# Kernel tuning notes

Hardware: AMD Instinct MI355X
Metric: run time of the kernel (lower is better)

Reference implementation:

```python
import jax, jax.numpy as jnp
import numpy as np

N, D, K = 65536, 256, 4096
INIT_COUNT = 100  # torch: counts = ones(K, int32) * 100


def setup_inputs() -> dict:
    key = jax.random.key(0)
    k1, k2 = jax.random.split(key)
    embedded = jax.random.normal(k1, (N, D), dtype=jnp.float32)
    centers = jax.random.normal(k2, (K, D), dtype=jnp.float32)
    counts = jnp.full((K,), INIT_COUNT, dtype=jnp.int32)
    return {"embedded": embedded, "centers": centers, "counts": counts}


def reference(embedded, centers, counts):
    # --- predict_hard: squared euclidean distance [N,K] + argmin ---
    x2 = jnp.sum(embedded * embedded, axis=1, keepdims=True)       # [N,1]
    c2 = jnp.sum(centers * centers, axis=1)                        # [K]
    d2 = x2 - 2.0 * (embedded @ centers.T) + c2                    # [N,K]
    labels = jnp.argmin(d2, axis=1).astype(jnp.int32)              # [N]

    # --- dcn_loss: mean over batch of squared dist to assigned center ---
    loss = jnp.sum((embedded - centers[labels]) ** 2) / embedded.shape[0]

    # --- update_centroids: sequential running-mean update, closed form ---
    # c <- (1-1/n)c + (1/n)x repeated over assigned samples collapses to
    # (count0 * c0 + sum_assigned x) / (count0 + m)
    seg_sum = jax.ops.segment_sum(embedded, labels, num_segments=K)            # [K,D]
    seg_cnt = jax.ops.segment_sum(
        jnp.ones((embedded.shape[0],), dtype=embedded.dtype), labels, num_segments=K
    )                                                                           # [K]
    c0 = counts.astype(embedded.dtype)                                          # [K]
    new_centers = (c0[:, None] * centers + seg_sum) / (c0 + seg_cnt)[:, None]  # [K,D]
    new_counts = counts + seg_cnt.astype(jnp.int32)                             # [K]
    return labels, new_centers, new_counts, loss
```

## Files before the change

### kernel.cpp

```cpp
#include <hip/hip_runtime.h>
#include <cfloat>
#include <cstdint>

constexpr int N  = 65536;
constexpr int D  = 256;
constexpr int K  = 4096;

typedef __attribute__((ext_vector_type(8))) _Float16 half8;
typedef __attribute__((ext_vector_type(8))) unsigned short ushort8;
typedef __attribute__((ext_vector_type(4))) float floatx4;

__device__ __forceinline__ floatx4 mfma_f16(half8 a, half8 b, floatx4 c) {
    return __builtin_amdgcn_mfma_f32_16x16x32_f16(a, b, c, 0, 0, 0);
}

__device__ __forceinline__ void ld_lds16(void* lds, const void* g) {
    __builtin_amdgcn_global_load_lds(
        (const __attribute__((address_space(1))) unsigned int*)g,
        (__attribute__((address_space(3))) unsigned int*)lds, 16, 0, 0);
}

__global__ void prep_c2(const float* __restrict__ C, float* __restrict__ c2) {
    int k = blockIdx.x;
    int l = threadIdx.x;
    const float4* row = (const float4*)(C + (size_t)k * D);
    float4 v = row[l];
    float s = v.x*v.x + v.y*v.y + v.z*v.z + v.w*v.w;
    #pragma unroll
    for (int m = 1; m < 64; m <<= 1) s += __shfl_xor(s, m);
    if (l == 0) c2[k] = s;
}

__global__ void convert_f16_both(const float* __restrict__ X, const float* __restrict__ C,
                                 unsigned short* __restrict__ Xh,
                                 unsigned short* __restrict__ Ch,
                                 float* __restrict__ xsq_part,
                                 float* __restrict__ c2) {
    __shared__ float red[4];
    int id = blockIdx.x * 256 + threadIdx.x;
    const int nX = N * D / 8;
    bool isX = id < nX;
    const float* src; unsigned short* dst;
    if (isX) { src = X; dst = Xh; }
    else     { src = C; dst = Ch; id -= nX; }
    const float4* s4 = (const float4*)src;
    float4 a = s4[2*id], b = s4[2*id+1];
    float xs[8] = {a.x,a.y,a.z,a.w,b.x,b.y,b.z,b.w};
    ushort8 h;
    float ps = 0.f;
    #pragma unroll
    for (int i = 0; i < 8; ++i) {
        union { _Float16 f; unsigned short u; } cv;
        cv.f = (_Float16)xs[i];
        h[i] = cv.u;
        ps += xs[i]*xs[i];
    }
    ((ushort8*)dst)[id] = h;
    int t = threadIdx.x;
    if (isX) {
        #pragma unroll
        for (int m = 1; m < 64; m <<= 1) ps += __shfl_xor(ps, m);
        if ((t & 63) == 0) red[t >> 6] = ps;
        __syncthreads();
        if (t == 0) xsq_part[blockIdx.x] = (red[0] + red[1]) + (red[2] + red[3]);
    } else {
        #pragma unroll
        for (int m = 1; m < 32; m <<= 1) ps += __shfl_xor(ps, m);
        if ((t & 31) == 0) c2[id >> 5] = ps;
    }
}

__global__ __launch_bounds__(256, 3) void mfma_assign(
        const unsigned short* __restrict__ Xh, const unsigned short* __restrict__ Ch,
        const float* __restrict__ c2g, float* __restrict__ cand)
{
    __shared__ __align__(16) unsigned short sA[2*8192];
    __shared__ __align__(16) unsigned short sB[2*4096];
    __shared__ float sC2[1024];

    const int t    = threadIdx.x;
    const int w    = t >> 6, l = t & 63;
    const int quad = l >> 4, lr = l & 15;

    const int bid   = blockIdx.x;
    const int sw    = (bid & 7) * 256 + (bid >> 3);
    const int kb    = sw & 3;
    const int panel = sw >> 2;
    const int rowbase = panel * 128;

    const int rl  = l >> 2;
    const int gsw = (l & 3) ^ ((l >> 3) & 3);

    ((float4*)sC2)[t] = ((const float4*)(c2g + kb*1024))[t];

#define STAGE(nk, db) do {                                                     \
        _Pragma("unroll")                                                      \
        for (int m_ = 0; m_ < 4; ++m_) {                                       \
            int dkk_ = m_ & 1, q_ = 2*w + (m_ >> 1);                           \
            const unsigned short* gp_ = Xh + (size_t)(rowbase + q_*16 + rl)*D  \
                + (((nk) & 3)*2 + dkk_)*32 + gsw*8;                            \
            ld_lds16((char*)sA + (db)*16384 + dkk_*8192 + q_*1024, gp_);       \
        }                                                                      \
        _Pragma("unroll")                                                      \
        for (int dkk_ = 0; dkk_ < 2; ++dkk_) {                                 \
            const unsigned short* gp_ = Ch + (size_t)(kb*1024 + ((nk)>>2)*64   \
                + w*16 + rl)*D + (((nk) & 3)*2 + dkk_)*32 + gsw*8;             \
            ld_lds16((char*)sB + (db)*8192 + dkk_*4096 + w*1024, gp_);         \
        }                                                                      \
    } while (0)

    STAGE(0, 0);

    const char* sAc = (const char*)sA;
    const char* sBc = (const char*)sB;
    const int slot   = quad ^ ((lr >> 1) & 3);
    const int sA_off = ((32*w + lr)*4 + slot)*16;
    const int sB_off = (lr*4 + slot)*16;

#define KSTEP(dkk) do {                                                        \
        const char* aB_ = sAc + buf*16384 + (dkk)*8192;                        \
        const char* bB_ = sBc + buf*8192  + (dkk)*4096;                        \
        half8 Af0 = *(const half8*)(aB_ + 0*1024 + sA_off);                    \
        half8 Af1 = *(const half8*)(aB_ + 1*1024 + sA_off);                    \
        half8 Bf0 = *(const half8*)(bB_ + 0*1024 + sB_off);                    \
        half8 Bf1 = *(const half8*)(bB_ + 1*1024 + sB_off);                    \
        half8 Bf2 = *(const half8*)(bB_ + 2*1024 + sB_off);                    \
        half8 Bf3 = *(const half8*)(bB_ + 3*1024 + sB_off);                    \
        acc[0][0] = mfma_f16(Af0, Bf0, acc[0][0]);                             \
        acc[1][0] = mfma_f16(Af1, Bf0, acc[1][0]);                             \
        acc[0][1] = mfma_f16(Af0, Bf1, acc[0][1]);                             \
        acc[1][1] = mfma_f16(Af1, Bf1, acc[1][1]);                             \
        acc[0][2] = mfma_f16(Af0, Bf2, acc[0][2]);                             \
        acc[1][2] = mfma_f16(Af1, Bf2, acc[1][2]);                             \
        acc[0][3] = mfma_f16(Af0, Bf3, acc[0][3]);                             \
        acc[1][3] = mfma_f16(Af1, Bf3, acc[1][3]);                             \
    } while (0)

#define FLUSH(h) do {                                                          \
    _Pragma("unroll")                                                          \
    for (int i = 0; i < 2; ++i)                                                \
        _Pragma("unroll")                                                      \
        for (int r = 0; r < 4; ++r) {                                          \
            int st = 4*i + r;                                                  \
            float a1 = v1[st], a2 = v2[st]; int ax1 = x1[st], ax2 = x2s[st];   \
            _Pragma("unroll")                                                  \
            for (int m = 1; m < 16; m <<= 1) {                                 \
                float b1f = __shfl_xor(a1, m); int bx1 = __shfl_xor(ax1, m);   \
                float b2f = __shfl_xor(a2, m); int bx2 = __shfl_xor(ax2, m);   \
                bool tt = (b1f < a1) || (b1f == a1 && bx1 < ax1);              \
                float n1 = tt ? b1f : a1; int nx1 = tt ? bx1 : ax1;            \
                float w1 = tt ? a1 : b1f; int wx1 = tt ? ax1 : bx1;            \
                float w2 = tt ? b2f : a2; int wx2 = tt ? bx2 : ax2;            \
                bool uu = (w2 < w1) || (w2 == w1 && wx2 < wx1);                \
                a1 = n1; ax1 = nx1;                                            \
                a2 = uu ? w2 : w1; ax2 = uu ? wx2 : wx1;                       \
            }                                                                  \
            if (lr == 0) {                                                     \
                int row = rowbase + 32*w + 16*i + 4*quad + r;                  \
                float4 o; o.x = a1; o.y = __int_as_float(ax1);                 \
                o.z = a2; o.w = __int_as_float(ax2);                           \
                ((float4*)cand)[(size_t)row*8 + (h)] = o;                      \
            }                                                                  \
            v1[st] = FLT_MAX; v2[st] = FLT_MAX;                                \
            x1[st] = 0x7fffffff; x2s[st] = 0x7fffffff;                         \
        } } while (0)

    float v1[8], v2[8]; int x1[8], x2s[8];
    #pragma unroll
    for (int i = 0; i < 8; ++i) { v1[i]=FLT_MAX; v2[i]=FLT_MAX; x1[i]=0x7fffffff; x2s[i]=0x7fffffff; }

    floatx4 acc[2][4];
    float c2v[4]; int jidx[4];
    int buf = 0;

    for (int ks = 0; ks < 64; ++ks) {
        __syncthreads();

        if (ks < 63) STAGE(ks + 1, buf ^ 1);

        if ((ks & 3) == 0) {
            const int ct = ks >> 2;
            #pragma unroll
            for (int i = 0; i < 2; ++i)
                #pragma unroll
                for (int j = 0; j < 4; ++j) acc[i][j] = (floatx4)0.f;
            #pragma unroll
            for (int j = 0; j < 4; ++j) {
                int cc = ct*64 + 16*j + lr;
                c2v[j] = sC2[cc];
                jidx[j] = kb*1024 + cc;
            }
        }

        KSTEP(0);
        KSTEP(1);

        if ((ks & 3) == 3) {
            #pragma unroll
            for (int i = 0; i < 2; ++i)
                #pragma unroll
                for (int j = 0; j < 4; ++j)
                    #pragma unroll
                    for (int r = 0; r < 4; ++r) {
                        float s = fmaf(-2.f, acc[i][j][r], c2v[j]);
                        int st = 4*i + r;
                        bool cA = s < v1[st];
                        bool cB = s < v2[st];
                        float tv = cB ? s : v2[st]; int tx = cB ? jidx[j] : x2s[st];
                        v2[st] = cA ? v1[st] : tv;  x2s[st] = cA ? x1[st] : tx;
                        v1[st] = cA ? s : v1[st];   x1[st]  = cA ? jidx[j] : x1[st];
                    }
        }
        if (ks == 31) FLUSH(2*kb);
        buf ^= 1;
    }
    FLUSH(2*kb + 1);

#undef STAGE
#undef KSTEP
#undef FLUSH
}

__global__ __launch_bounds__(256) void recheck_label(
        const float* __restrict__ X, const float* __restrict__ C,
        const float* __restrict__ c2, const float* __restrict__ cand,
        float* __restrict__ out_labels, int* __restrict__ labInt,
        int* __restrict__ cnt)
{
    int t = threadIdx.x, w = t >> 6, l = t & 63;
    int g  = l >> 4;
    int lr = l & 15;
    int row0 = (blockIdx.x * 4 + w) * 4;
    int row  = row0 + g;

    float4 e = ((const float4*)cand)[(size_t)row*8 + (lr >> 1)];
    float s  = (lr & 1) ? e.z : e.x;
    int  idx = (lr & 1) ? __float_as_int(e.w) : __float_as_int(e.y);

    float a1 = s, a2 = FLT_MAX; int ax1 = idx, ax2 = 0x7fffffff;
    #pragma unroll
    for (int m = 1; m < 16; m <<= 1) {
        float b1 = __shfl_xor(a1, m); int bx1 = __shfl_xor(ax1, m);
        float b2 = __shfl_xor(a2, m); int bx2 = __shfl_xor(ax2, m);
        bool tt = (b1 < a1) || (b1 == a1 && bx1 < ax1);
        float n1 = tt ? b1 : a1; int nx1 = tt ? bx1 : ax1;
        float w1 = tt ? a1 : b1; int wx1 = tt ? ax1 : bx1;
        float w2 = tt ? b2 : a2; int wx2 = tt ? bx2 : ax2;
        bool uu = (w2 < w1) || (w2 == w1 && wx2 < wx1);
        a1 = n1; ax1 = nx1;
        a2 = uu ? w2 : w1; ax2 = uu ? wx2 : wx1;
    }

    bool certain = (a2 - a1 > 0.25f);
    unsigned long long certMask = __ballot(certain);

    if (certain && lr == 0) {
        out_labels[row] = (float)ax1;
        labInt[row] = ax1;
        atomicAdd(&cnt[ax1], 1);
    }

    #pragma unroll
    for (int q = 0; q < 4; ++q) {
        if ((certMask >> (q*16)) & 1ull) continue;
        int r = row0 + q;
        float sq  = __shfl(s,   q*16 + lr);
        int   iq  = __shfl(idx, q*16 + lr);
        float gs1 = __shfl(a1,  q*16);

        float4 xv = ((const float4*)X)[(size_t)r*64 + l];
        float px = xv.x*xv.x + xv.y*xv.y + xv.z*xv.z + xv.w*xv.w;
        #pragma unroll
        for (int m = 1; m < 64; m <<= 1) px += __shfl_xor(px, m);

        bool active = (l < 16) && (sq <= gs1 + 0.25f);
        unsigned long long mask = __ballot(active);
        float best = FLT_MAX; int bi = 0x7fffffff;
        while (mask) {
            int k = __ffsll((long long)mask) - 1;
            mask &= mask - 1;
            int ck = __shfl(iq, k);
            float4 cv = ((const float4*)C)[(size_t)ck*64 + l];
            float pd = xv.x*cv.x + xv.y*cv.y + xv.z*cv.z + xv.w*cv.w;
            #pragma unroll
            for (int m = 1; m < 64; m <<= 1) pd += __shfl_xor(pd, m);
            float d2 = fmaf(-2.f, pd, px) + c2[ck];
            if (d2 < best || (d2 == best && ck < bi)) { best = d2; bi = ck; }
        }
        if (l == 0) {
            out_labels[r] = (float)bi;
            labInt[r] = bi;
            atomicAdd(&cnt[bi], 1);
        }
    }
}

__global__ void prefix_kernel(const int* __restrict__ cnt,
                              int* __restrict__ offs, int* __restrict__ cursor) {
    int l = threadIdx.x;
    int s = 0;
    #pragma unroll 8
    for (int i = 0; i < 64; ++i) s += cnt[l*64 + i];
    int inc = s;
    #pragma unroll
    for (int off = 1; off < 64; off <<= 1) {
        int u = __shfl_up(inc, off);
        if (l >= off) inc += u;
    }
    int run = inc - s;
    for (int i = 0; i < 64; ++i) {
        int k = l*64 + i;
        offs[k] = run; cursor[k] = run;
        run += cnt[k];
    }
}

__global__ void scatter_idx(const int* __restrict__ labInt,
                            int* __restrict__ cursor, int* __restrict__ sortedIdx) {
    int i = blockIdx.x * 256 + threadIdx.x;
    int lab = labInt[i];
    int pos = atomicAdd(&cursor[lab], 1);
    sortedIdx[pos] = i;
}

__global__ __launch_bounds__(256) void center_update(
        const float* __restrict__ X, const float* __restrict__ C,
        const int* __restrict__ counts0, const int* __restrict__ cnt,
        const int* __restrict__ offs, const int* __restrict__ sortedIdx,
        float* __restrict__ lossC, float* __restrict__ out)
{
    __shared__ float red[4];
    int k = blockIdx.x, d = threadIdx.x;
    int start = offs[k], m = cnt[k];
    float acc = 0.f;
    int i = 0;
    for (; i + 4 <= m; i += 4) {
        int r0 = sortedIdx[start+i],   r1 = sortedIdx[start+i+1];
        int r2 = sortedIdx[start+i+2], r3 = sortedIdx[start+i+3];
        float a0 = X[(size_t)r0*D + d], a1 = X[(size_t)r1*D + d];
        float a2 = X[(size_t)r2*D + d], a3 = X[(size_t)r3*D + d];
        acc += (a0 + a1) + (a2 + a3);
    }
    for (; i < m; ++i) acc += X[(size_t)sortedIdx[start+i]*D + d];

    float cv = C[(size_t)k*D + d];
    float c0 = (float)counts0[k];
    out[N + (size_t)k*D + d] = (c0 * cv + acc) / (c0 + (float)m);
    if (d == 0) out[N + (size_t)K*D + k] = (float)(counts0[k] + m);

    float lp = cv * fmaf((float)m, cv, -2.f*acc);
    #pragma unroll
    for (int s = 1; s < 64; s <<= 1) lp += __shfl_xor(lp, s);
    if ((d & 63) == 0) red[d >> 6] = lp;
    __syncthreads();
    if (d == 0) lossC[k] = (red[0] + red[1]) + (red[2] + red[3]);
}

__global__ __launch_bounds__(256) void loss_final(
        const float* __restrict__ xsq_part, const float* __restrict__ lossC,
        float* __restrict__ out)
{
    __shared__ double red[4];
    int t = threadIdx.x;
    double s = 0.0;
    for (int i = t; i < 8192; i += 256) s += (double)xsq_part[i];
    for (int i = t; i < 4096; i += 256) s += (double)lossC[i];
    #pragma unroll
    for (int m = 1; m < 64; m <<= 1) s += __shfl_xor(s, m);
    if ((t & 63) == 0) red[t >> 6] = s;
    __syncthreads();
    if (t == 0)
        out[N + (size_t)K*D + K] = (float)(((red[0] + red[1]) + (red[2] + red[3])) / (double)N);
}

__global__ void finalize_kernel(const float* __restrict__ C,
                                const int* __restrict__ counts0,
                                const float* __restrict__ seg,
                                const int* __restrict__ cnt,
                                const double* __restrict__ lossAcc,
                                float* __restrict__ out)
{
    int g = blockIdx.x * 256 + threadIdx.x;
    int k = g >> 8;
    float c0 = (float)counts0[k];
    float m  = (float)cnt[k];
    out[N + g] = (c0 * C[g] + seg[g]) / (c0 + m);
    if (g < K) out[N + (size_t)K*D + g] = (float)(counts0[g] + cnt[g]);
    if (g == 0) out[N + (size_t)K*D + K] = (float)(lossAcc[0] / (double)N);
}

__global__ __launch_bounds__(256, 2) void assign_fp32(
        const float* __restrict__ X, const float* __restrict__ C,
        const float* __restrict__ c2, float* __restrict__ out_labels,
        float* __restrict__ seg, int* __restrict__ cnt,
        double* __restrict__ lossAcc)
{
    constexpr int BM = 128, BN = 128, KD = 16;
    __shared__ float As[KD][BM];
    __shared__ float Bs[KD][BN];
    __shared__ float x2f[BM];
    __shared__ int   labs[BM];

    const int t  = threadIdx.x;
    const int tx = t & 15;
    const int ty = t >> 4;
    const int rowbase = blockIdx.x * BM;

    {
        int r  = t >> 1;
        int dh = (t & 1) * (D / 2);
        const float4* xr = (const float4*)(X + (size_t)(rowbase + r) * D + dh);
        float s = 0.f;
        #pragma unroll
        for (int i = 0; i < D / 8; ++i) {
            float4 v = xr[i];
            s += v.x*v.x + v.y*v.y + v.z*v.z + v.w*v.w;
        }
        s += __shfl_xor(s, 1);
        if ((t & 1) == 0) x2f[r] = s;
    }
    __syncthreads();

    float x2v[8];
    #pragma unroll
    for (int i = 0; i < 4; ++i) { x2v[i] = x2f[4*ty + i]; x2v[i+4] = x2f[64 + 4*ty + i]; }

    float rmv[8]; int rmi[8];
    #pragma unroll
    for (int i = 0; i < 8; ++i) { rmv[i] = FLT_MAX; rmi[i] = 0x7fffffff; }

    for (int ct = 0; ct < K / BN; ++ct) {
        float acc[8][8];
        #pragma unroll
        for (int i = 0; i < 8; ++i)
            #pragma unroll
            for (int j = 0; j < 8; ++j) acc[i][j] = 0.f;

        float c2f2[8];
        {
            float4 a = *(const float4*)(c2 + ct*BN + 4*tx);
            float4 b = *(const float4*)(c2 + ct*BN + 64 + 4*tx);
            c2f2[0]=a.x; c2f2[1]=a.y; c2f2[2]=a.z; c2f2[3]=a.w;
            c2f2[4]=b.x; c2f2[5]=b.y; c2f2[6]=b.z; c2f2[7]=b.w;
        }

        for (int dk = 0; dk < D / KD; ++dk) {
            #pragma unroll
            for (int i = 0; i < 2; ++i) {
                int f  = t + 256 * i;
                int r  = f >> 2;
                int dp = f & 3;
                float4 av = *(const float4*)(X + (size_t)(rowbase + r) * D + dk*KD + 4*dp);
                float4 bv = *(const float4*)(C + (size_t)(ct*BN + r) * D + dk*KD + 4*dp);
                As[4*dp+0][r]=av.x; As[4*dp+1][r]=av.y; As[4*dp+2][r]=av.z; As[4*dp+3][r]=av.w;
                Bs[4*dp+0][r]=bv.x; Bs[4*dp+1][r]=bv.y; Bs[4*dp+2][r]=bv.z; Bs[4*dp+3][r]=bv.w;
            }
            __syncthreads();
            #pragma unroll
            for (int kk = 0; kk < KD; ++kk) {
                float4 a0 = *(const float4*)&As[kk][4*ty];
                float4 a1 = *(const float4*)&As[kk][64 + 4*ty];
                float4 b0 = *(const float4*)&Bs[kk][4*tx];
                float4 b1 = *(const float4*)&Bs[kk][64 + 4*tx];
                float av[8] = {a0.x,a0.y,a0.z,a0.w,a1.x,a1.y,a1.z,a1.w};
                float bv[8] = {b0.x,b0.y,b0.z,b0.w,b1.x,b1.y,b1.z,b1.w};
                #pragma unroll
                for (int i = 0; i < 8; ++i)
                    #pragma unroll
                    for (int j = 0; j < 8; ++j)
                        acc[i][j] = fmaf(av[i], bv[j], acc[i][j]);
            }
            __syncthreads();
        }

        #pragma unroll
        for (int i = 0; i < 8; ++i) {
            float bv = FLT_MAX; int bi = 0x7fffffff;
            #pragma unroll
            for (int j = 0; j < 8; ++j) {
                int coll = (j < 4) ? (4*tx + j) : (64 + 4*tx + (j - 4));
                float v = fmaf(-2.f, acc[i][j], x2v[i]) + c2f2[j];
                int idx = ct * BN + coll;
                if (v < bv || (v == bv && idx < bi)) { bv = v; bi = idx; }
            }
            #pragma unroll
            for (int m = 1; m < 16; m <<= 1) {
                float ov = __shfl_xor(bv, m);
                int   oi = __shfl_xor(bi, m);
                if (ov < bv || (ov == bv && oi < bi)) { bv = ov; bi = oi; }
            }
            if (bv < rmv[i] || (bv == rmv[i] && bi < rmi[i])) { rmv[i] = bv; rmi[i] = bi; }
        }
    }

    if (tx == 0) {
        #pragma unroll
        for (int i = 0; i < 8; ++i) {
            int r = (i < 4) ? (4*ty + i) : (64 + 4*ty + (i - 4));
            labs[r] = rmi[i];
            out_labels[rowbase + r] = (float)rmi[i];
            atomicAdd(&cnt[rmi[i]], 1);
        }
    }
    __syncthreads();

    {
        int r   = t >> 1;
        int dh  = (t & 1) * (D / 2);
        int lab = labs[r];
        const float4* xr = (const float4*)(X + (size_t)(rowbase + r) * D + dh);
        const float4* cr = (const float4*)(C + (size_t)lab * D + dh);
        float* sp = seg + (size_t)lab * D + dh;
        float ls = 0.f;
        #pragma unroll 8
        for (int i = 0; i < D / 8; ++i) {
            float4 xv = xr[i];
            float4 cv = cr[i];
            atomicAdd(sp + 4*i + 0, xv.x);
            atomicAdd(sp + 4*i + 1, xv.y);
            atomicAdd(sp + 4*i + 2, xv.z);
            atomicAdd(sp + 4*i + 3, xv.w);
            float d0 = xv.x - cv.x, d1 = xv.y - cv.y;
            float d2 = xv.z - cv.z, d3 = xv.w - cv.w;
            ls += d0*d0 + d1*d1 + d2*d2 + d3*d3;
        }
        #pragma unroll
        for (int m = 1; m < 64; m <<= 1) ls += __shfl_xor(ls, m);
        if ((t & 63) == 0) atomicAdd(lossAcc, (double)ls);
    }
}

extern "C" void kernel_launch(void* const* d_in, const int* in_sizes, int n_in,
                              void* d_out, int out_size, void* d_ws, size_t ws_size,
                              hipStream_t stream) {
    const float* X       = (const float*)d_in[0];
    const float* C       = (const float*)d_in[1];
    const int*   counts0 = (const int*)d_in[2];
    float* out = (float*)d_out;

    char* p = (char*)d_ws;
    float*  seg     = (float*)p;          p += (size_t)K * D * 4;
    int*    cnt     = (int*)p;            p += (size_t)K * 4;
    float*  c2      = (float*)p;          p += (size_t)K * 4;
    double* lossAcc = (double*)p;         p += 16;
    size_t zero_all = (size_t)(p - (char*)d_ws);
    float*  cand    = (float*)p;          p += (size_t)N * 32 * 4;
    unsigned short* Xh = (unsigned short*)p; p += (size_t)N * D * 2;
    unsigned short* Ch = (unsigned short*)p; p += (size_t)K * D * 2;
    float* xsq_part = (float*)p;          p += 8192 * 4;
    float* lossC    = (float*)p;          p += (size_t)K * 4;
    size_t need = (size_t)(p - (char*)d_ws);

    int* labInt    = (int*)seg;
    int* sortedIdx = labInt + N;
    int* offs      = sortedIdx + N;
    int* cursor    = offs + K;

    if (ws_size >= need) {
        hipMemsetAsync(cnt, 0, (size_t)K * 4, stream);
        convert_f16_both<<<(N*D/8 + K*D/8)/256, 256, 0, stream>>>(X, C, Xh, Ch, xsq_part, c2);
        mfma_assign<<<2048, 256, 0, stream>>>(Xh, Ch, c2, cand);
        recheck_label<<<N/16, 256, 0, stream>>>(X, C, c2, cand, out, labInt, cnt);
        prefix_kernel<<<1, 64, 0, stream>>>(cnt, offs, cursor);
        scatter_idx<<<N/256, 256, 0, stream>>>(labInt, cursor, sortedIdx);
        center_update<<<K, 256, 0, stream>>>(X, C, counts0, cnt, offs, sortedIdx, lossC, out);
        loss_final<<<1, 256, 0, stream>>>(xsq_part, lossC, out);
    } else {
        hipMemsetAsync(d_ws, 0, zero_all, stream);
        prep_c2<<<K, 64, 0, stream>>>(C, c2);
        assign_fp32<<<N/128, 256, 0, stream>>>(X, C, c2, out, seg, cnt, lossAcc);
        finalize_kernel<<<(K*D)/256, 256, 0, stream>>>(C, counts0, seg, cnt, lossAcc, out);
    }
}
```

Measured before the change: 588.4 us.

## Split centroid range across 8 blocks per row panel with smaller K-step tiles

Each block of the MFMA assignment kernel now handles 512 centroids instead of 1024, so twice as many blocks are launched. The staged depth chunk per step is halved (one 32-wide slice instead of two), which shrinks LDS use and raises occupancy to 4 blocks per SM. The per-block c2 preload into shared memory is dropped in favour of direct global reads. The cost is more blocks re-reading the same X panel and more per-step sync and loop overhead.

```diff
diff --git a/kernel.cpp b/kernel.cpp
--- a/kernel.cpp
+++ b/kernel.cpp
@@ -70,42 +70,38 @@
     }
 }
 
-__global__ __launch_bounds__(256, 3) void mfma_assign(
+__global__ __launch_bounds__(256, 4) void mfma_assign(
         const unsigned short* __restrict__ Xh, const unsigned short* __restrict__ Ch,
         const float* __restrict__ c2g, float* __restrict__ cand)
 {
-    __shared__ __align__(16) unsigned short sA[2*8192];
-    __shared__ __align__(16) unsigned short sB[2*4096];
-    __shared__ float sC2[1024];
+    __shared__ __align__(16) unsigned short sA[2*4096];
+    __shared__ __align__(16) unsigned short sB[2*2048];
 
     const int t    = threadIdx.x;
     const int w    = t >> 6, l = t & 63;
     const int quad = l >> 4, lr = l & 15;
 
     const int bid   = blockIdx.x;
-    const int sw    = (bid & 7) * 256 + (bid >> 3);
-    const int kb    = sw & 3;
-    const int panel = sw >> 2;
+    const int sw    = (bid & 7) * 512 + (bid >> 3);
+    const int kb8   = sw & 7;
+    const int panel = sw >> 3;
     const int rowbase = panel * 128;
 
     const int rl  = l >> 2;
     const int gsw = (l & 3) ^ ((l >> 3) & 3);
 
-    ((float4*)sC2)[t] = ((const float4*)(c2g + kb*1024))[t];
-
 #define STAGE(nk, db) do {                                                     \
         _Pragma("unroll")                                                      \
-        for (int m_ = 0; m_ < 4; ++m_) {                                       \
-            int dkk_ = m_ & 1, q_ = 2*w + (m_ >> 1);                           \
+        for (int m_ = 0; m_ < 2; ++m_) {                                       \
+            int q_ = 2*w + m_;                                                 \
             const unsigned short* gp_ = Xh + (size_t)(rowbase + q_*16 + rl)*D  \
-                + (((nk) & 3)*2 + dkk_)*32 + gsw*8;                            \
-            ld_lds16((char*)sA + (db)*16384 + dkk_*8192 + q_*1024, gp_);       \
+                + ((nk) & 7)*32 + gsw*8;                                       \
+            ld_lds16((char*)sA + (db)*8192 + q_*1024, gp_);                    \
         }                                                                      \
-        _Pragma("unroll")                                                      \
-        for (int dkk_ = 0; dkk_ < 2; ++dkk_) {                                 \
-            const unsigned short* gp_ = Ch + (size_t)(kb*1024 + ((nk)>>2)*64   \
-                + w*16 + rl)*D + (((nk) & 3)*2 + dkk_)*32 + gsw*8;             \
-            ld_lds16((char*)sB + (db)*8192 + dkk_*4096 + w*1024, gp_);         \
+        {                                                                      \
+            const unsigned short* gp_ = Ch + (size_t)(kb8*512 + ((nk)>>3)*64   \
+                + w*16 + rl)*D + ((nk) & 7)*32 + gsw*8;                        \
+            ld_lds16((char*)sB + (db)*4096 + w*1024, gp_);                     \
         }                                                                      \
     } while (0)
 
@@ -117,9 +113,9 @@
     const int sA_off = ((32*w + lr)*4 + slot)*16;
     const int sB_off = (lr*4 + slot)*16;
 
-#define KSTEP(dkk) do {                                                        \
-        const char* aB_ = sAc + buf*16384 + (dkk)*8192;                        \
-        const char* bB_ = sBc + buf*8192  + (dkk)*4096;                        \
+#define KSTEP() do {                                                           \
+        const char* aB_ = sAc + buf*8192;                                      \
+        const char* bB_ = sBc + buf*4096;                                      \
         half8 Af0 = *(const half8*)(aB_ + 0*1024 + sA_off);                    \
         half8 Af1 = *(const half8*)(aB_ + 1*1024 + sA_off);                    \
         half8 Bf0 = *(const half8*)(bB_ + 0*1024 + sB_off);                    \
@@ -161,8 +157,6 @@
                 o.z = a2; o.w = __int_as_float(ax2);                           \
                 ((float4*)cand)[(size_t)row*8 + (h)] = o;                      \
             }                                                                  \
-            v1[st] = FLT_MAX; v2[st] = FLT_MAX;                                \
-            x1[st] = 0x7fffffff; x2s[st] = 0x7fffffff;                         \
         } } while (0)
 
     float v1[8], v2[8]; int x1[8], x2s[8];
@@ -178,24 +172,23 @@
 
         if (ks < 63) STAGE(ks + 1, buf ^ 1);
 
-        if ((ks & 3) == 0) {
-            const int ct = ks >> 2;
+        if ((ks & 7) == 0) {
+            const int ct = ks >> 3;
             #pragma unroll
             for (int i = 0; i < 2; ++i)
                 #pragma unroll
                 for (int j = 0; j < 4; ++j) acc[i][j] = (floatx4)0.f;
             #pragma unroll
             for (int j = 0; j < 4; ++j) {
-                int cc = ct*64 + 16*j + lr;
-                c2v[j] = sC2[cc];
-                jidx[j] = kb*1024 + cc;
+                int col = kb8*512 + ct*64 + 16*j + lr;
+                c2v[j] = c2g[col];
+                jidx[j] = col;
             }
         }
 
-        KSTEP(0);
-        KSTEP(1);
-
-        if ((ks & 3) == 3) {
+        KSTEP();
+
+        if ((ks & 7) == 7) {
             #pragma unroll
             for (int i = 0; i < 2; ++i)
                 #pragma unroll
@@ -211,10 +204,9 @@
                         v1[st] = cA ? s : v1[st];   x1[st]  = cA ? jidx[j] : x1[st];
                     }
         }
-        if (ks == 31) FLUSH(2*kb);
         buf ^= 1;
     }
-    FLUSH(2*kb + 1);
+    FLUSH(kb8);
 
 #undef STAGE
 #undef KSTEP
@@ -559,7 +551,7 @@
     if (ws_size >= need) {
         hipMemsetAsync(cnt, 0, (size_t)K * 4, stream);
         convert_f16_both<<<(N*D/8 + K*D/8)/256, 256, 0, stream>>>(X, C, Xh, Ch, xsq_part, c2);
-        mfma_assign<<<2048, 256, 0, stream>>>(Xh, Ch, c2, cand);
+        mfma_assign<<<4096, 256, 0, stream>>>(Xh, Ch, c2, cand);
         recheck_label<<<N/16, 256, 0, stream>>>(X, C, c2, cand, out, labInt, cnt);
         prefix_kernel<<<1, 64, 0, stream>>>(cnt, offs, cursor);
         scatter_idx<<<N/256, 256, 0, stream>>>(labInt, cursor, sortedIdx);
```

Result: slower. 631.5 us (+7.3%).
